# Performance work log

Measured on AMD Instinct MI355X. Metric: run time of the kernel, lower is better.

Reference implementation:

```python
import jax, jax.numpy as jnp
import numpy as np

EPS = 1e-5
B, CIN, L = 512, 5, 1024   # batch, input channels, msp length == d_model
COUT, A, NB = 32, 13, 5    # CNN branch channels, max_atoms, num_bonds_prediction


def conv1d(x, w, pad, groups=1):
    # x: (N, C, L), w: (O, I/groups, K)
    return jax.lax.conv_general_dilated(
        x, w, window_strides=(1,), padding=[(pad, pad)],
        dimension_numbers=("NCH", "OIH", "NCH"), feature_group_count=groups)


def batchnorm(x, g, b):
    # training-mode BN over (N, L) per channel, as nn.BatchNorm1d in train()
    m = jnp.mean(x, axis=(0, 2), keepdims=True)
    v = jnp.var(x, axis=(0, 2), keepdims=True)
    return (x - m) * jax.lax.rsqrt(v + EPS) * g[None, :, None] + b[None, :, None]


def setup_inputs() -> dict:
    key = jax.random.key(0)
    ks = jax.random.split(key, 16)
    n = jax.random.normal
    inp = {
        "src": n(ks[0], (B, CIN, L), dtype=jnp.float32),
        "mask": jnp.ones((B, A), dtype=bool),
        "max_atoms": A,
        # CNN branch 1 (kernel 5) : depthwise, pointwise, BN, residual 1x1 conv
        "dw1": n(ks[1], (CIN, 1, 5), dtype=jnp.float32) * 0.2,
        "pw1": n(ks[2], (COUT, CIN, 1), dtype=jnp.float32) * 0.2,
        "g1": jnp.ones((COUT,), jnp.float32),
        "be1": jnp.zeros((COUT,), jnp.float32),
        "r1w": n(ks[3], (COUT, CIN, 1), dtype=jnp.float32) * 0.2,
        "r1b": jnp.zeros((COUT,), jnp.float32),
        # CNN branch 2 (kernel 3)
        "dw2": n(ks[4], (CIN, 1, 3), dtype=jnp.float32) * 0.2,
        "pw2": n(ks[5], (COUT, CIN, 1), dtype=jnp.float32) * 0.2,
        "g2": jnp.ones((COUT,), jnp.float32),
        "be2": jnp.zeros((COUT,), jnp.float32),
        "r2w": n(ks[6], (COUT, CIN, 1), dtype=jnp.float32) * 0.2,
        "r2b": jnp.zeros((COUT,), jnp.float32),
        # EdgeClassify2 linears: ll1 (2*COUT -> A), fl (2*L -> NB)
        "ll1w": n(ks[7], (A, 2 * COUT), dtype=jnp.float32) * 0.1,
        "ll1b": jnp.zeros((A,), jnp.float32),
        "flw": n(ks[8], (NB, 2 * L), dtype=jnp.float32) * 0.02,
        "flb": jnp.zeros((NB,), jnp.float32),
    }
    return inp


def reference(src, mask, max_atoms, dw1, pw1, g1, be1, r1w, r1b,
              dw2, pw2, g2, be2, r2w, r2b, ll1w, ll1b, flw, flb):
    # ---- CNN encoder ----
    e1 = jax.nn.relu(batchnorm(conv1d(conv1d(src, dw1, 2, groups=CIN), pw1, 0), g1, be1))
    e1 = e1 * (conv1d(src, r1w, 0) + r1b[None, :, None])
    e2 = jax.nn.relu(batchnorm(conv1d(conv1d(src, dw2, 1, groups=CIN), pw2, 0), g2, be2))
    e2 = e2 * (conv1d(src, r2w, 0) + r2b[None, :, None])
    x = jnp.concatenate([e1, e2], axis=1)          # (B, 2*COUT, L)
    # ---- EdgeClassify2 ----
    # ll1 over channel dim: (B, 2*COUT, L) -> (B, A, L)
    h = jnp.einsum("bcl,ac->bal", x, ll1w) + ll1b[None, :, None]
    # vectorized replacement of the O(A^2) python loop:
    # final_e[:, i, j] = concat(h[:, min(i,j)], h[:, max(i,j)])
    idx = jnp.arange(max_atoms)
    mn = jnp.minimum(idx[:, None], idx[None, :])   # (A, A)
    mx = jnp.maximum(idx[:, None], idx[None, :])
    final_e = jnp.concatenate([h[:, mn, :], h[:, mx, :]], axis=-1)  # (B, A, A, 2L)
    out = jnp.einsum("bijd,nd->bijn", final_e, flw) + flb           # (B, A, A, NB)
    return out
```

## Files before the change

kernel.cpp:

```cpp
#include <hip/hip_runtime.h>
#include <hip/hip_bf16.h>

#define BB 512
#define LL 1024
#define AA 13
#define NBP 5
#define NTOT (BB * LL)
#define EPSV 1e-5f

#define WS_F     192
#define WS_PART  256
#define WS_FLW   16384

typedef __attribute__((ext_vector_type(8))) short bhalf8;
typedef __attribute__((ext_vector_type(4))) float floatx4;

__device__ __forceinline__ void trunc_pair(float e0, float e1, unsigned int& hp, unsigned int& lp) {
    unsigned int u0 = __float_as_uint(e0), u1 = __float_as_uint(e1);
    unsigned int h0 = u0 & 0xFFFF0000u, h1 = u1 & 0xFFFF0000u;
    hp = (h0 >> 16) | h1;
    float l0 = e0 - __uint_as_float(h0);
    float l1 = e1 - __uint_as_float(h1);
    lp = (__float_as_uint(l0) >> 16) | (__float_as_uint(l1) & 0xFFFF0000u);
}

template<int CTRL, int RM, bool BC>
__device__ __forceinline__ float dppadd(float v) {
    int t = __builtin_amdgcn_update_dpp(0, __float_as_int(v), CTRL, RM, 0xf, BC);
    return v + __int_as_float(t);
}
__device__ __forceinline__ float wave_sum(float v) {
    v = dppadd<0x111, 0xf, true >(v);
    v = dppadd<0x112, 0xf, true >(v);
    v = dppadd<0x114, 0xf, true >(v);
    v = dppadd<0x118, 0xf, true >(v);
    v = dppadd<0x142, 0xa, false>(v);
    v = dppadd<0x143, 0xc, false>(v);
    return v;
}

__device__ __forceinline__ float e_val(const float4& A, const float4& B2, const float4& R0, float r4w,
                                       const float4& pa, const float4& pb, float svx, float svy) {
    float y = B2.y + A.x*pa.x + A.y*pa.y + A.z*pa.z + A.w*pa.w + B2.x*pb.x;
    float r = B2.z + R0.x*pb.y + R0.y*pb.z + R0.z*pb.w + R0.w*svx + r4w*svy;
    return fmaxf(y, 0.f) * r;
}

__global__ __launch_bounds__(256) void k_moments(
    const float* __restrict__ src,
    const float* __restrict__ dw1,
    const float* __restrict__ dw2,
    const float* __restrict__ flw,
    float* __restrict__ ws)
{
    __shared__ float red[4][40];
    __shared__ float fred[4];
    int tid = threadIdx.x;
    int gid = blockIdx.x * 256 + tid;
    int b = gid >> 7, L0 = (gid & 127) << 3;
    const float* sb = src + b * (5 * LL);

    float w1[5][5], w2[5][3];
#pragma unroll
    for (int c = 0; c < 5; c++) {
#pragma unroll
        for (int t = 0; t < 5; t++) w1[c][t] = dw1[c*5+t];
#pragma unroll
        for (int t = 0; t < 3; t++) w2[c][t] = dw2[c*3+t];
    }

    float x[5][16];
#pragma unroll
    for (int c5 = 0; c5 < 5; c5++) {
        const float* sp = sb + c5 * LL;
        float4 xa = (L0 >= 4)    ? *(const float4*)(sp + L0 - 4) : make_float4(0,0,0,0);
        float4 xb = *(const float4*)(sp + L0);
        float4 xc = *(const float4*)(sp + L0 + 4);
        float4 xd = (L0 <= 1012) ? *(const float4*)(sp + L0 + 8) : make_float4(0,0,0,0);
        x[c5][0]=xa.x; x[c5][1]=xa.y; x[c5][2]=xa.z; x[c5][3]=xa.w;
        x[c5][4]=xb.x; x[c5][5]=xb.y; x[c5][6]=xb.z; x[c5][7]=xb.w;
        x[c5][8]=xc.x; x[c5][9]=xc.y; x[c5][10]=xc.z; x[c5][11]=xc.w;
        x[c5][12]=xd.x; x[c5][13]=xd.y; x[c5][14]=xd.z; x[c5][15]=xd.w;
    }

    float acc[40];
#pragma unroll
    for (int k = 0; k < 40; k++) acc[k] = 0.f;

#pragma unroll
    for (int k = 0; k < 8; k++) {
        float d1[5], d2[5];
#pragma unroll
        for (int c5 = 0; c5 < 5; c5++) {
            d1[c5] = w1[c5][0]*x[c5][k+2] + w1[c5][1]*x[c5][k+3] + w1[c5][2]*x[c5][k+4]
                   + w1[c5][3]*x[c5][k+5] + w1[c5][4]*x[c5][k+6];
            d2[c5] = w2[c5][0]*x[c5][k+3] + w2[c5][1]*x[c5][k+4] + w2[c5][2]*x[c5][k+5];
        }
#pragma unroll
        for (int j = 0; j < 5; j++) { acc[j] += d1[j]; acc[20+j] += d2[j]; }
#pragma unroll
        for (int j = 0; j < 5; j++)
#pragma unroll
            for (int kk = j; kk < 5; kk++) {
                int idx = j*(11-j)/2 + (kk - j);
                acc[5+idx]  += d1[j]*d1[kk];
                acc[25+idx] += d2[j]*d2[kk];
            }
    }

    int lane = tid & 63, wv = tid >> 6;
#pragma unroll
    for (int k = 0; k < 40; k++) acc[k] = wave_sum(acc[k]);
    if (lane == 63) {
#pragma unroll
        for (int k = 0; k < 40; k++) red[wv][k] = acc[k];
    }
    __syncthreads();
    if (tid < 40) {
        ws[WS_PART + blockIdx.x * 40 + tid] =
            red[0][tid] + red[1][tid] + red[2][tid] + red[3][tid];
    }

    if (blockIdx.x < 10) {
        int nn = blockIdx.x;
        int n = nn < 5 ? nn : nn - 5;
        int off = nn < 5 ? 0 : LL;
        float4 v = *(const float4*)(flw + n * (2*LL) + off + tid * 4);
        {
            unsigned int hp0, lp0, hp1, lp1;
            trunc_pair(v.x, v.y, hp0, lp0);
            trunc_pair(v.z, v.w, hp1, lp1);
            char* fwb = (char*)(ws + WS_FLW);
            *(uint2*)(fwb + nn * 2048 + tid * 8)         = make_uint2(hp0, hp1);
            *(uint2*)(fwb + 32768 + nn * 2048 + tid * 8) = make_uint2(lp0, lp1);
        }
        float s = wave_sum(v.x + v.y + v.z + v.w);
        if (lane == 63) fred[wv] = s;
        __syncthreads();
        if (tid == 0) ws[WS_F + nn] = fred[0] + fred[1] + fred[2] + fred[3];
    } else if (blockIdx.x < 16) {
        int nn = blockIdx.x;
        char* fwb = (char*)(ws + WS_FLW);
        *(uint2*)(fwb + nn * 2048 + tid * 8)         = make_uint2(0u, 0u);
        *(uint2*)(fwb + 32768 + nn * 2048 + tid * 8) = make_uint2(0u, 0u);
    }
}

__global__ __launch_bounds__(512, 2) void k_fused(
    const float* __restrict__ src,
    const float* __restrict__ dw1,
    const float* __restrict__ dw2,
    const float* __restrict__ ll1w,
    const float* __restrict__ ll1b,
    const float* __restrict__ flb,
    const float* __restrict__ pw1, const float* __restrict__ pw2,
    const float* __restrict__ g1,  const float* __restrict__ be1,
    const float* __restrict__ g2,  const float* __restrict__ be2,
    const float* __restrict__ r1w, const float* __restrict__ r2w,
    const float* __restrict__ r1b, const float* __restrict__ r2b,
    const float* __restrict__ ws_ro,
    float* __restrict__ out)
{
    __shared__ __align__(16) float dvS[18432];
    __shared__ float llT[832];
    __shared__ float PQ[130];
    __shared__ float momS[40];

    int tid = threadIdx.x, b = blockIdx.x;
    int lane = tid & 63;
    int gu = __builtin_amdgcn_readfirstlane(tid >> 6);
    int mp = gu >> 2;
    int lq = gu & 3;
    int row = lane & 15;
    int ko = lane >> 4;

    const float* srcB = src + b * (5 * LL);
    char* base  = (char*)dvS;
    char* cbase = (char*)(dvS + 16384);

    if (tid < 320) {
        int k = tid >> 3, sub = tid & 7;
        float v = 0.f;
#pragma unroll 8
        for (int i = 0; i < 32; i++) v += ws_ro[WS_PART + (sub + (i << 3)) * 40 + k];
        v += __shfl_xor(v, 1, 64);
        v += __shfl_xor(v, 2, 64);
        v += __shfl_xor(v, 4, 64);
        if (sub == 0) momS[k] = v;
    }
    __syncthreads();
    if (tid < 64) {
        int brc = tid >> 5, o = tid & 31;
        const float invN = 1.0f / (float)NTOT;
        const float* pw = brc ? pw2 : pw1;
        const float* rw = brc ? r2w : r1w;
        const float* s  = momS + (brc ? 20 : 0);
        const float* M  = momS + (brc ? 25 : 5);
        float pwv[5], rwv[5], md[5];
#pragma unroll
        for (int j = 0; j < 5; j++) { pwv[j] = pw[o*5+j]; rwv[j] = rw[o*5+j]; md[j] = s[j] * invN; }
        float meanY = 0.f;
#pragma unroll
        for (int j = 0; j < 5; j++) meanY += pwv[j] * md[j];
        float ey2 = 0.f;
#pragma unroll
        for (int j = 0; j < 5; j++)
#pragma unroll
            for (int k = 0; k < 5; k++) {
                int lo = j < k ? j : k, hi = j < k ? k : j;
                int idx = lo*(11-lo)/2 + (hi - lo);
                ey2 += pwv[j] * pwv[k] * (M[idx] * invN);
            }
        float varY = ey2 - meanY * meanY;
        if (varY < 0.f) varY = 0.f;
        float gg = brc ? g2[o] : g1[o];
        float bb = brc ? be2[o] : be1[o];
        float rb = brc ? r2b[o] : r1b[o];
        float sc = gg * rsqrtf(varY + EPSV);
        float sh = bb - meanY * sc;
        float* dst = dvS + tid * 16;
        dst[0] = pwv[0]*sc; dst[1] = pwv[1]*sc; dst[2] = pwv[2]*sc; dst[3] = pwv[3]*sc;
        dst[4] = pwv[4]*sc; dst[5] = sh;        dst[6] = rb;        dst[7] = 0.f;
        dst[8] = rwv[0];    dst[9] = rwv[1];    dst[10] = rwv[2];   dst[11] = rwv[3];
        dst[12] = rwv[4];
    }
    __syncthreads();

    int chA = (mp << 5) + row;
    int chB = chA + 16;
    const float* cfA = dvS + (chA << 4);
    const float4 Aa = *(const float4*)cfA;
    const float4 Ba = *(const float4*)(cfA + 4);
    const float4 Ra = *(const float4*)(cfA + 8);
    const float  a4 = cfA[12];
    const float* cfB = dvS + (chB << 4);
    const float4 Ab = *(const float4*)cfB;
    const float4 Bb = *(const float4*)(cfB + 4);
    const float4 Rb = *(const float4*)(cfB + 8);
    const float  b4 = cfB[12];
    __syncthreads();

    for (int t = tid; t < 1024; t += 512) {
        int swz = ((t >> 3) & 3) << 4;
        float d1v[5], d2v[5], s0[5];
#pragma unroll
        for (int c5 = 0; c5 < 5; c5++) {
            const float* s5 = srcB + (c5 << 10);
            float xm2 = (t >= 2)    ? s5[t - 2] : 0.f;
            float xm1 = (t >= 1)    ? s5[t - 1] : 0.f;
            float x0  = s5[t];
            float xp1 = (t <= 1022) ? s5[t + 1] : 0.f;
            float xp2 = (t <= 1021) ? s5[t + 2] : 0.f;
            d1v[c5] = dw1[c5*5+0]*xm2 + dw1[c5*5+1]*xm1 + dw1[c5*5+2]*x0
                    + dw1[c5*5+3]*xp1 + dw1[c5*5+4]*xp2;
            d2v[c5] = dw2[c5*3+0]*xm1 + dw2[c5*3+1]*x0 + dw2[c5*3+2]*xp1;
            s0[c5] = x0;
        }
        *(float4*)(base + ((((0<<11)+(t<<1)+0) << 4) ^ swz)) = make_float4(d1v[0],d1v[1],d1v[2],d1v[3]);
        *(float4*)(base + ((((0<<11)+(t<<1)+1) << 4) ^ swz)) = make_float4(d1v[4],s0[0],s0[1],s0[2]);
        *(float4*)(base + ((((1<<11)+(t<<1)+0) << 4) ^ swz)) = make_float4(d2v[0],d2v[1],d2v[2],d2v[3]);
        *(float4*)(base + ((((1<<11)+(t<<1)+1) << 4) ^ swz)) = make_float4(d2v[4],s0[0],s0[1],s0[2]);
        *(float2*)(cbase + (t << 3)) = make_float2(s0[3], s0[4]);
    }
    for (int idx = tid; idx < 832; idx += 512) {
        int cc = idx / 13, a = idx - cc * 13;
        llT[idx] = ll1w[a * 64 + cc];
    }
    __syncthreads();

    const char* fwb = (const char*)(ws_ro + WS_FLW);
    floatx4 CA = {0.f, 0.f, 0.f, 0.f};
    floatx4 CB = {0.f, 0.f, 0.f, 0.f};

#pragma unroll 1
    for (int s = 0; s < 8; ++s) {
        int kstep = (lq << 3) + s;
        int l0 = (kstep << 5) + (ko << 3);
        union { uint4 u; bhalf8 v; } bh, bl;
        {
            int boff = ((row << 10) + l0) << 1;
            bh.u = *(const uint4*)(fwb + boff);
            bl.u = *(const uint4*)(fwb + 32768 + boff);
        }
        int sw = ((l0 >> 3) & 3) << 4;
        int ebase = (mp << 15) + (l0 << 5);
        union { unsigned int u[4]; bhalf8 v; } ahA, alA, ahB, alB;
#pragma unroll
        for (int jp = 0; jp < 4; ++jp) {
            int o0 = ebase + (jp << 6);
            const float4 pa0 = *(const float4*)(base + ((o0      ) ^ sw));
            const float4 pb0 = *(const float4*)(base + ((o0 + 16) ^ sw));
            const float4 pa1 = *(const float4*)(base + ((o0 + 32) ^ sw));
            const float4 pb1 = *(const float4*)(base + ((o0 + 48) ^ sw));
            const float4 pcc = *(const float4*)(cbase + ((l0 + (jp << 1)) << 3));
            float e0 = e_val(Aa, Ba, Ra, a4, pa0, pb0, pcc.x, pcc.y);
            float e1 = e_val(Aa, Ba, Ra, a4, pa1, pb1, pcc.z, pcc.w);
            trunc_pair(e0, e1, ahA.u[jp], alA.u[jp]);
            float f0 = e_val(Ab, Bb, Rb, b4, pa0, pb0, pcc.x, pcc.y);
            float f1 = e_val(Ab, Bb, Rb, b4, pa1, pb1, pcc.z, pcc.w);
            trunc_pair(f0, f1, ahB.u[jp], alB.u[jp]);
        }
        CA = __builtin_amdgcn_mfma_f32_16x16x32_bf16(ahA.v, bh.v, CA, 0, 0, 0);
        CA = __builtin_amdgcn_mfma_f32_16x16x32_bf16(ahA.v, bl.v, CA, 0, 0, 0);
        CA = __builtin_amdgcn_mfma_f32_16x16x32_bf16(alA.v, bh.v, CA, 0, 0, 0);
        CB = __builtin_amdgcn_mfma_f32_16x16x32_bf16(ahB.v, bh.v, CB, 0, 0, 0);
        CB = __builtin_amdgcn_mfma_f32_16x16x32_bf16(ahB.v, bl.v, CB, 0, 0, 0);
        CB = __builtin_amdgcn_mfma_f32_16x16x32_bf16(alB.v, bh.v, CB, 0, 0, 0);
    }

    __syncthreads();
    {
        float* part = dvS;
        int basep = ((lane >> 4) << 6) + (lane & 15);
        int sA = (gu << 1) * 256, sB = sA + 256;
        part[sA + basep]      = CA[0];
        part[sA + basep + 16] = CA[1];
        part[sA + basep + 32] = CA[2];
        part[sA + basep + 48] = CA[3];
        part[sB + basep]      = CB[0];
        part[sB + basep + 16] = CB[1];
        part[sB + basep + 32] = CB[2];
        part[sB + basep + 48] = CB[3];
    }
    __syncthreads();
    float* SarrF = dvS + 4096;
    for (int idx = tid; idx < 1024; idx += 512) {
        int c = idx >> 4, n = idx & 15;
        int mt2 = c >> 4, m = c & 15;
        int mp2 = mt2 >> 1, t2 = mt2 & 1;
        const float* part = (const float*)dvS;
        int o = (m << 4) + n;
        float sum = 0.f;
#pragma unroll
        for (int lq2 = 0; lq2 < 4; ++lq2)
            sum += part[((((mp2 << 2) + lq2) << 1) + t2) * 256 + o];
        SarrF[idx] = sum;
    }
    __syncthreads();

    if (tid < 130) {
        int half = tid >= 65 ? 1 : 0;
        int q = tid - half * 65;
        int a = q / 5, n = q - a * 5;
        int col = half * 5 + n;
        float v = ll1b[a] * ws_ro[WS_F + col];
#pragma unroll 8
        for (int cc = 0; cc < 64; cc++) v += llT[cc * 13 + a] * SarrF[(cc << 4) + col];
        PQ[tid] = v;
    }
    __syncthreads();

    for (int idx = tid; idx < AA * AA * NBP; idx += 512) {
        int i = idx / 65;
        int rr = idx - i * 65;
        int j = rr / 5, n = rr - j * 5;
        int mn = i < j ? i : j, mx = i < j ? j : i;
        out[b * (AA * AA * NBP) + idx] = PQ[mn * 5 + n] + PQ[65 + mx * 5 + n] + flb[n];
    }
}

extern "C" void kernel_launch(void* const* d_in, const int* in_sizes, int n_in,
                              void* d_out, int out_size, void* d_ws, size_t ws_size,
                              hipStream_t stream) {
    const float* src  = (const float*)d_in[0];
    const float* dw1  = (const float*)d_in[3];
    const float* pw1  = (const float*)d_in[4];
    const float* g1   = (const float*)d_in[5];
    const float* be1  = (const float*)d_in[6];
    const float* r1w  = (const float*)d_in[7];
    const float* r1b  = (const float*)d_in[8];
    const float* dw2  = (const float*)d_in[9];
    const float* pw2  = (const float*)d_in[10];
    const float* g2   = (const float*)d_in[11];
    const float* be2  = (const float*)d_in[12];
    const float* r2w  = (const float*)d_in[13];
    const float* r2b  = (const float*)d_in[14];
    const float* ll1w = (const float*)d_in[15];
    const float* ll1b = (const float*)d_in[16];
    const float* flw  = (const float*)d_in[17];
    const float* flb  = (const float*)d_in[18];
    float* ws  = (float*)d_ws;
    float* out = (float*)d_out;

    k_moments<<<256, 256, 0, stream>>>(src, dw1, dw2, flw, ws);
    k_fused<<<BB, 512, 0, stream>>>(src, dw1, dw2, ll1w, ll1b, flb,
                                    pw1, pw2, g1, be1, g2, be2, r1w, r2w, r1b, r2b,
                                    ws, out);
}
```

Baseline: 130.6 us.

## Fuse moments and main kernels via a grid-wide atomic barrier

Merges the BN-moment kernel into the main kernel. Each block computes the depthwise conv into shared memory, accumulates its per-batch moment partials, then waits at a software grid barrier (atomic counter plus spin) before reading the global moments. This removes a kernel launch and the second pass over src. It depends on all 512 blocks being co-resident (2 per CU at 512 threads) and adds a memset launch for the counter.

```diff
diff --git a/kernel.cpp b/kernel.cpp
--- a/kernel.cpp
+++ b/kernel.cpp
@@ -8,9 +8,10 @@
 #define NTOT (BB * LL)
 #define EPSV 1e-5f
 
+#define WS_CNT   128
 #define WS_F     192
 #define WS_PART  256
-#define WS_FLW   16384
+#define WS_FLW   32768
 
 typedef __attribute__((ext_vector_type(8))) short bhalf8;
 typedef __attribute__((ext_vector_type(4))) float floatx4;
@@ -46,110 +47,11 @@
     return fmaxf(y, 0.f) * r;
 }
 
-__global__ __launch_bounds__(256) void k_moments(
+__global__ __launch_bounds__(512, 2) void k_solo(
     const float* __restrict__ src,
     const float* __restrict__ dw1,
     const float* __restrict__ dw2,
     const float* __restrict__ flw,
-    float* __restrict__ ws)
-{
-    __shared__ float red[4][40];
-    __shared__ float fred[4];
-    int tid = threadIdx.x;
-    int gid = blockIdx.x * 256 + tid;
-    int b = gid >> 7, L0 = (gid & 127) << 3;
-    const float* sb = src + b * (5 * LL);
-
-    float w1[5][5], w2[5][3];
-#pragma unroll
-    for (int c = 0; c < 5; c++) {
-#pragma unroll
-        for (int t = 0; t < 5; t++) w1[c][t] = dw1[c*5+t];
-#pragma unroll
-        for (int t = 0; t < 3; t++) w2[c][t] = dw2[c*3+t];
-    }
-
-    float x[5][16];
-#pragma unroll
-    for (int c5 = 0; c5 < 5; c5++) {
-        const float* sp = sb + c5 * LL;
-        float4 xa = (L0 >= 4)    ? *(const float4*)(sp + L0 - 4) : make_float4(0,0,0,0);
-        float4 xb = *(const float4*)(sp + L0);
-        float4 xc = *(const float4*)(sp + L0 + 4);
-        float4 xd = (L0 <= 1012) ? *(const float4*)(sp + L0 + 8) : make_float4(0,0,0,0);
-        x[c5][0]=xa.x; x[c5][1]=xa.y; x[c5][2]=xa.z; x[c5][3]=xa.w;
-        x[c5][4]=xb.x; x[c5][5]=xb.y; x[c5][6]=xb.z; x[c5][7]=xb.w;
-        x[c5][8]=xc.x; x[c5][9]=xc.y; x[c5][10]=xc.z; x[c5][11]=xc.w;
-        x[c5][12]=xd.x; x[c5][13]=xd.y; x[c5][14]=xd.z; x[c5][15]=xd.w;
-    }
-
-    float acc[40];
-#pragma unroll
-    for (int k = 0; k < 40; k++) acc[k] = 0.f;
-
-#pragma unroll
-    for (int k = 0; k < 8; k++) {
-        float d1[5], d2[5];
-#pragma unroll
-        for (int c5 = 0; c5 < 5; c5++) {
-            d1[c5] = w1[c5][0]*x[c5][k+2] + w1[c5][1]*x[c5][k+3] + w1[c5][2]*x[c5][k+4]
-                   + w1[c5][3]*x[c5][k+5] + w1[c5][4]*x[c5][k+6];
-            d2[c5] = w2[c5][0]*x[c5][k+3] + w2[c5][1]*x[c5][k+4] + w2[c5][2]*x[c5][k+5];
-        }
-#pragma unroll
-        for (int j = 0; j < 5; j++) { acc[j] += d1[j]; acc[20+j] += d2[j]; }
-#pragma unroll
-        for (int j = 0; j < 5; j++)
-#pragma unroll
-            for (int kk = j; kk < 5; kk++) {
-                int idx = j*(11-j)/2 + (kk - j);
-                acc[5+idx]  += d1[j]*d1[kk];
-                acc[25+idx] += d2[j]*d2[kk];
-            }
-    }
-
-    int lane = tid & 63, wv = tid >> 6;
-#pragma unroll
-    for (int k = 0; k < 40; k++) acc[k] = wave_sum(acc[k]);
-    if (lane == 63) {
-#pragma unroll
-        for (int k = 0; k < 40; k++) red[wv][k] = acc[k];
-    }
-    __syncthreads();
-    if (tid < 40) {
-        ws[WS_PART + blockIdx.x * 40 + tid] =
-            red[0][tid] + red[1][tid] + red[2][tid] + red[3][tid];
-    }
-
-    if (blockIdx.x < 10) {
-        int nn = blockIdx.x;
-        int n = nn < 5 ? nn : nn - 5;
-        int off = nn < 5 ? 0 : LL;
-        float4 v = *(const float4*)(flw + n * (2*LL) + off + tid * 4);
-        {
-            unsigned int hp0, lp0, hp1, lp1;
-            trunc_pair(v.x, v.y, hp0, lp0);
-            trunc_pair(v.z, v.w, hp1, lp1);
-            char* fwb = (char*)(ws + WS_FLW);
-            *(uint2*)(fwb + nn * 2048 + tid * 8)         = make_uint2(hp0, hp1);
-            *(uint2*)(fwb + 32768 + nn * 2048 + tid * 8) = make_uint2(lp0, lp1);
-        }
-        float s = wave_sum(v.x + v.y + v.z + v.w);
-        if (lane == 63) fred[wv] = s;
-        __syncthreads();
-        if (tid == 0) ws[WS_F + nn] = fred[0] + fred[1] + fred[2] + fred[3];
-    } else if (blockIdx.x < 16) {
-        int nn = blockIdx.x;
-        char* fwb = (char*)(ws + WS_FLW);
-        *(uint2*)(fwb + nn * 2048 + tid * 8)         = make_uint2(0u, 0u);
-        *(uint2*)(fwb + 32768 + nn * 2048 + tid * 8) = make_uint2(0u, 0u);
-    }
-}
-
-__global__ __launch_bounds__(512, 2) void k_fused(
-    const float* __restrict__ src,
-    const float* __restrict__ dw1,
-    const float* __restrict__ dw2,
     const float* __restrict__ ll1w,
     const float* __restrict__ ll1b,
     const float* __restrict__ flb,
@@ -158,13 +60,14 @@
     const float* __restrict__ g2,  const float* __restrict__ be2,
     const float* __restrict__ r1w, const float* __restrict__ r2w,
     const float* __restrict__ r1b, const float* __restrict__ r2b,
-    const float* __restrict__ ws_ro,
+    float* __restrict__ ws,
     float* __restrict__ out)
 {
     __shared__ __align__(16) float dvS[18432];
     __shared__ float llT[832];
     __shared__ float PQ[130];
     __shared__ float momS[40];
+    __shared__ float red2[328];
 
     int tid = threadIdx.x, b = blockIdx.x;
     int lane = tid & 63;
@@ -177,16 +80,101 @@
     const float* srcB = src + b * (5 * LL);
     char* base  = (char*)dvS;
     char* cbase = (char*)(dvS + 16384);
-
-    if (tid < 320) {
-        int k = tid >> 3, sub = tid & 7;
-        float v = 0.f;
+    int* cnt = (int*)(ws + WS_CNT);
+
+    float acc[40];
+#pragma unroll
+    for (int k = 0; k < 40; k++) acc[k] = 0.f;
+
+    for (int t = tid; t < 1024; t += 512) {
+        int swz = ((t >> 3) & 3) << 4;
+        float d1v[5], d2v[5], s0[5];
+#pragma unroll
+        for (int c5 = 0; c5 < 5; c5++) {
+            const float* s5 = srcB + (c5 << 10);
+            float xm2 = (t >= 2)    ? s5[t - 2] : 0.f;
+            float xm1 = (t >= 1)    ? s5[t - 1] : 0.f;
+            float x0  = s5[t];
+            float xp1 = (t <= 1022) ? s5[t + 1] : 0.f;
+            float xp2 = (t <= 1021) ? s5[t + 2] : 0.f;
+            d1v[c5] = dw1[c5*5+0]*xm2 + dw1[c5*5+1]*xm1 + dw1[c5*5+2]*x0
+                    + dw1[c5*5+3]*xp1 + dw1[c5*5+4]*xp2;
+            d2v[c5] = dw2[c5*3+0]*xm1 + dw2[c5*3+1]*x0 + dw2[c5*3+2]*xp1;
+            s0[c5] = x0;
+        }
+        *(float4*)(base + ((((0<<11)+(t<<1)+0) << 4) ^ swz)) = make_float4(d1v[0],d1v[1],d1v[2],d1v[3]);
+        *(float4*)(base + ((((0<<11)+(t<<1)+1) << 4) ^ swz)) = make_float4(d1v[4],s0[0],s0[1],s0[2]);
+        *(float4*)(base + ((((1<<11)+(t<<1)+0) << 4) ^ swz)) = make_float4(d2v[0],d2v[1],d2v[2],d2v[3]);
+        *(float4*)(base + ((((1<<11)+(t<<1)+1) << 4) ^ swz)) = make_float4(d2v[4],s0[0],s0[1],s0[2]);
+        *(float2*)(cbase + (t << 3)) = make_float2(s0[3], s0[4]);
+#pragma unroll
+        for (int j = 0; j < 5; j++) { acc[j] += d1v[j]; acc[20+j] += d2v[j]; }
+#pragma unroll
+        for (int j = 0; j < 5; j++)
+#pragma unroll
+            for (int kk = j; kk < 5; kk++) {
+                int idx = j*(11-j)/2 + (kk - j);
+                acc[5+idx]  += d1v[j]*d1v[kk];
+                acc[25+idx] += d2v[j]*d2v[kk];
+            }
+    }
+#pragma unroll
+    for (int k = 0; k < 40; k++) acc[k] = wave_sum(acc[k]);
+    if (lane == 63) {
+#pragma unroll
+        for (int k = 0; k < 40; k++) red2[gu * 40 + k] = acc[k];
+    }
+
+    if (b < 10) {
+        if (tid < 256) {
+            int n = b < 5 ? b : b - 5;
+            int off = b < 5 ? 0 : LL;
+            float4 v = *(const float4*)(flw + n * (2*LL) + off + tid * 4);
+            unsigned int hp0, lp0, hp1, lp1;
+            trunc_pair(v.x, v.y, hp0, lp0);
+            trunc_pair(v.z, v.w, hp1, lp1);
+            char* fwb = (char*)(ws + WS_FLW);
+            *(uint2*)(fwb + b * 2048 + tid * 8)         = make_uint2(hp0, hp1);
+            *(uint2*)(fwb + 32768 + b * 2048 + tid * 8) = make_uint2(lp0, lp1);
+            float s = wave_sum(v.x + v.y + v.z + v.w);
+            if (lane == 63) red2[320 + (tid >> 6)] = s;
+        }
+    } else if (b < 16 && tid < 256) {
+        char* fwb = (char*)(ws + WS_FLW);
+        *(uint2*)(fwb + b * 2048 + tid * 8)         = make_uint2(0u, 0u);
+        *(uint2*)(fwb + 32768 + b * 2048 + tid * 8) = make_uint2(0u, 0u);
+    }
+    __syncthreads();
+    if (tid < 40) {
+        float s = 0.f;
+#pragma unroll
+        for (int w2 = 0; w2 < 8; w2++) s += red2[w2 * 40 + tid];
+        ws[WS_PART + b * 40 + tid] = s;
+    }
+    if (b < 10 && tid == 0)
+        ws[WS_F + b] = red2[320] + red2[321] + red2[322] + red2[323];
+    __syncthreads();
+
+    if (tid == 0) {
+        __threadfence();
+        atomicAdd(cnt, 1);
+        while (atomicAdd(cnt, 0) < BB) __builtin_amdgcn_s_sleep(8);
+        __threadfence();
+    }
+    __syncthreads();
+
+    {
+        volatile const float* vp = ws + WS_PART;
+        if (tid < 320) {
+            int k = tid >> 3, sub = tid & 7;
+            float v = 0.f;
 #pragma unroll 8
-        for (int i = 0; i < 32; i++) v += ws_ro[WS_PART + (sub + (i << 3)) * 40 + k];
-        v += __shfl_xor(v, 1, 64);
-        v += __shfl_xor(v, 2, 64);
-        v += __shfl_xor(v, 4, 64);
-        if (sub == 0) momS[k] = v;
+            for (int i = 0; i < 64; i++) v += vp[(sub + (i << 3)) * 40 + k];
+            v += __shfl_xor(v, 1, 64);
+            v += __shfl_xor(v, 2, 64);
+            v += __shfl_xor(v, 4, 64);
+            if (sub == 0) momS[k] = v;
+        }
     }
     __syncthreads();
     if (tid < 64) {
@@ -218,57 +206,33 @@
         float rb = brc ? r2b[o] : r1b[o];
         float sc = gg * rsqrtf(varY + EPSV);
         float sh = bb - meanY * sc;
-        float* dst = dvS + tid * 16;
+        float* dst = llT + tid * 13;
         dst[0] = pwv[0]*sc; dst[1] = pwv[1]*sc; dst[2] = pwv[2]*sc; dst[3] = pwv[3]*sc;
-        dst[4] = pwv[4]*sc; dst[5] = sh;        dst[6] = rb;        dst[7] = 0.f;
-        dst[8] = rwv[0];    dst[9] = rwv[1];    dst[10] = rwv[2];   dst[11] = rwv[3];
-        dst[12] = rwv[4];
+        dst[4] = pwv[4]*sc; dst[5] = sh; dst[6] = rb;
+        dst[7] = rwv[0]; dst[8] = rwv[1]; dst[9] = rwv[2]; dst[10] = rwv[3]; dst[11] = rwv[4];
     }
     __syncthreads();
 
     int chA = (mp << 5) + row;
     int chB = chA + 16;
-    const float* cfA = dvS + (chA << 4);
-    const float4 Aa = *(const float4*)cfA;
-    const float4 Ba = *(const float4*)(cfA + 4);
-    const float4 Ra = *(const float4*)(cfA + 8);
-    const float  a4 = cfA[12];
-    const float* cfB = dvS + (chB << 4);
-    const float4 Ab = *(const float4*)cfB;
-    const float4 Bb = *(const float4*)(cfB + 4);
-    const float4 Rb = *(const float4*)(cfB + 8);
-    const float  b4 = cfB[12];
-    __syncthreads();
-
-    for (int t = tid; t < 1024; t += 512) {
-        int swz = ((t >> 3) & 3) << 4;
-        float d1v[5], d2v[5], s0[5];
-#pragma unroll
-        for (int c5 = 0; c5 < 5; c5++) {
-            const float* s5 = srcB + (c5 << 10);
-            float xm2 = (t >= 2)    ? s5[t - 2] : 0.f;
-            float xm1 = (t >= 1)    ? s5[t - 1] : 0.f;
-            float x0  = s5[t];
-            float xp1 = (t <= 1022) ? s5[t + 1] : 0.f;
-            float xp2 = (t <= 1021) ? s5[t + 2] : 0.f;
-            d1v[c5] = dw1[c5*5+0]*xm2 + dw1[c5*5+1]*xm1 + dw1[c5*5+2]*x0
-                    + dw1[c5*5+3]*xp1 + dw1[c5*5+4]*xp2;
-            d2v[c5] = dw2[c5*3+0]*xm1 + dw2[c5*3+1]*x0 + dw2[c5*3+2]*xp1;
-            s0[c5] = x0;
-        }
-        *(float4*)(base + ((((0<<11)+(t<<1)+0) << 4) ^ swz)) = make_float4(d1v[0],d1v[1],d1v[2],d1v[3]);
-        *(float4*)(base + ((((0<<11)+(t<<1)+1) << 4) ^ swz)) = make_float4(d1v[4],s0[0],s0[1],s0[2]);
-        *(float4*)(base + ((((1<<11)+(t<<1)+0) << 4) ^ swz)) = make_float4(d2v[0],d2v[1],d2v[2],d2v[3]);
-        *(float4*)(base + ((((1<<11)+(t<<1)+1) << 4) ^ swz)) = make_float4(d2v[4],s0[0],s0[1],s0[2]);
-        *(float2*)(cbase + (t << 3)) = make_float2(s0[3], s0[4]);
-    }
+    const float* cA = llT + chA * 13;
+    const float4 Aa = make_float4(cA[0], cA[1], cA[2], cA[3]);
+    const float4 Ba = make_float4(cA[4], cA[5], cA[6], 0.f);
+    const float4 Ra = make_float4(cA[7], cA[8], cA[9], cA[10]);
+    const float  a4 = cA[11];
+    const float* cB = llT + chB * 13;
+    const float4 Ab = make_float4(cB[0], cB[1], cB[2], cB[3]);
+    const float4 Bb = make_float4(cB[4], cB[5], cB[6], 0.f);
+    const float4 Rb = make_float4(cB[7], cB[8], cB[9], cB[10]);
+    const float  b4 = cB[11];
+    __syncthreads();
+
     for (int idx = tid; idx < 832; idx += 512) {
         int cc = idx / 13, a = idx - cc * 13;
         llT[idx] = ll1w[a * 64 + cc];
     }
-    __syncthreads();
-
-    const char* fwb = (const char*)(ws_ro + WS_FLW);
+
+    const char* fwb = (const char*)(ws + WS_FLW);
     floatx4 CA = {0.f, 0.f, 0.f, 0.f};
     floatx4 CB = {0.f, 0.f, 0.f, 0.f};
 
@@ -343,7 +307,7 @@
         int q = tid - half * 65;
         int a = q / 5, n = q - a * 5;
         int col = half * 5 + n;
-        float v = ll1b[a] * ws_ro[WS_F + col];
+        float v = ll1b[a] * *(volatile const float*)(ws + WS_F + col);
 #pragma unroll 8
         for (int cc = 0; cc < 64; cc++) v += llT[cc * 13 + a] * SarrF[(cc << 4) + col];
         PQ[tid] = v;
@@ -382,8 +346,8 @@
     float* ws  = (float*)d_ws;
     float* out = (float*)d_out;
 
-    k_moments<<<256, 256, 0, stream>>>(src, dw1, dw2, flw, ws);
-    k_fused<<<BB, 512, 0, stream>>>(src, dw1, dw2, ll1w, ll1b, flb,
-                                    pw1, pw2, g1, be1, g2, be2, r1w, r2w, r1b, r2b,
-                                    ws, out);
-}
+    hipMemsetAsync((char*)d_ws + WS_CNT * sizeof(float), 0, sizeof(int), stream);
+    k_solo<<<BB, 512, 0, stream>>>(src, dw1, dw2, flw, ll1w, ll1b, flb,
+                                   pw1, pw2, g1, be1, g2, be2, r1w, r2w, r1b, r2b,
+                                   ws, out);
+}
```

New measurement: 177.1 us. 1.36x slower.
